# Kernel optimization log

Measured on AMD Instinct MI355X. Metric: run time of the kernel, lower is better.

## Reference

```python
import jax, jax.numpy as jnp
import numpy as np
import math

B, T, C = 2, 2048, 2048
H, KV, HD = 16, 4, 128  # num_heads, num_kv_heads, head_dim
REP = H // KV


def _rope_tables(T, hd, base=10000.0):
    inv_freq = 1.0 / (base ** (np.arange(0, hd, 2, dtype=np.float32) / hd))  # [hd/2]
    t = np.arange(T, dtype=np.float32)
    freqs = np.outer(t, inv_freq)                 # [T, hd/2]
    emb = np.concatenate([freqs, freqs], axis=-1)  # [T, hd]
    return jnp.asarray(np.cos(emb)), jnp.asarray(np.sin(emb))


def setup_inputs() -> dict:
    key = jax.random.key(0)
    ks = jax.random.split(key, 5)
    cos, sin = _rope_tables(T, HD)
    std = 0.02
    return {
        "x": jax.random.normal(ks[0], (B, T, C), dtype=jnp.float32),
        "cos": cos,
        "sin": sin,
        "Wq": jax.random.normal(ks[1], (C, H * HD), dtype=jnp.float32) * std,
        "Wk": jax.random.normal(ks[2], (C, KV * HD), dtype=jnp.float32) * std,
        "Wv": jax.random.normal(ks[3], (C, KV * HD), dtype=jnp.float32) * std,
        "Wo": jax.random.normal(ks[4], (H * HD, C), dtype=jnp.float32) * std,
    }


def _rotate_half(t):
    h = t.shape[-1] // 2
    return jnp.concatenate([-t[..., h:], t[..., :h]], axis=-1)


def reference(x, cos, sin, Wq, Wk, Wv, Wo):
    Bx, Tx, Cx = x.shape
    q = (x @ Wq).reshape(Bx, Tx, H, HD).transpose(0, 2, 1, 3)   # [B,H,T,hd]
    k = (x @ Wk).reshape(Bx, Tx, KV, HD).transpose(0, 2, 1, 3)  # [B,KV,T,hd]
    v = (x @ Wv).reshape(Bx, Tx, KV, HD).transpose(0, 2, 1, 3)
    c = cos[None, None]  # [1,1,T,hd]
    s = sin[None, None]
    q = q * c + _rotate_half(q) * s
    k = k * c + _rotate_half(k) * s
    # repeat_kv: expand KV heads to H heads (interleave within groups)
    k = jnp.repeat(k, REP, axis=1)  # [B,H,T,hd]
    v = jnp.repeat(v, REP, axis=1)
    scores = jnp.einsum("bhqd,bhkd->bhqk", q, k) / math.sqrt(HD)
    causal = jnp.triu(jnp.full((Tx, Tx), float("-inf"), dtype=scores.dtype), k=1)
    scores = jax.nn.softmax(scores + causal[None, None], axis=-1)
    out = jnp.einsum("bhqk,bhkd->bhqd", scores, v)  # [B,H,T,hd]
    out = out.transpose(0, 2, 1, 3).reshape(Bx, Tx, H * HD)
    return out @ Wo
```

## Files before the change

kernel.cpp:

```cpp
#include <hip/hip_runtime.h>
#include <hip/hip_bf16.h>
#include <math.h>

typedef __bf16 bf16_t;
typedef __bf16 bf16x8 __attribute__((ext_vector_type(8)));
typedef float f32x4 __attribute__((ext_vector_type(4)));

constexpr int Bc = 2, Tc = 2048, Cdim = 2048, Hc = 16, KVc = 4, HDc = 128;
constexpr int Mc = Bc * Tc;
constexpr int Nqkv = 3072;

typedef const __attribute__((address_space(1))) void* as1_cptr;
typedef __attribute__((address_space(3))) void* as3_ptr;

__device__ __forceinline__ void gload_lds16(const bf16_t* g, bf16_t* l) {
  __builtin_amdgcn_global_load_lds((as1_cptr)(const void*)g, (as3_ptr)(void*)l, 16, 0, 0);
}

__global__ void k_cvt_bf16(const float* __restrict__ in, bf16_t* __restrict__ out) {
  int i = (blockIdx.x * 256 + threadIdx.x) * 8;
  float4 a = *(const float4*)(in + i);
  float4 b = *(const float4*)(in + i + 4);
  bf16x8 v;
  v[0] = (bf16_t)a.x; v[1] = (bf16_t)a.y; v[2] = (bf16_t)a.z; v[3] = (bf16_t)a.w;
  v[4] = (bf16_t)b.x; v[5] = (bf16_t)b.y; v[6] = (bf16_t)b.z; v[7] = (bf16_t)b.w;
  *(bf16x8*)(out + i) = v;
}

__global__ void k_w_trans(const float* __restrict__ W, bf16_t* __restrict__ Wt,
                          int K, int N) {
  __shared__ alignas(16) bf16_t tile[64][72];
  const int k0 = blockIdx.x * 64, n0 = blockIdx.y * 64;
  const int t = threadIdx.x;
#pragma unroll
  for (int i = 0; i < 4; ++i) {
    int idx = t + i * 256;
    int r = idx >> 4;
    int c4 = (idx & 15) * 4;
    float4 v = *(const float4*)(W + (size_t)(k0 + r) * N + n0 + c4);
    tile[r][c4 + 0] = (bf16_t)v.x; tile[r][c4 + 1] = (bf16_t)v.y;
    tile[r][c4 + 2] = (bf16_t)v.z; tile[r][c4 + 3] = (bf16_t)v.w;
  }
  __syncthreads();
#pragma unroll
  for (int i = 0; i < 4; ++i) {
    int idx = t + i * 256;
    int n = idx >> 4;
    int kc = (idx & 15) * 4;
    alignas(8) bf16_t o[4];
#pragma unroll
    for (int j = 0; j < 4; ++j) o[j] = tile[kc + j][n];
    *(uint2*)(Wt + (size_t)(n0 + n) * K + k0 + kc) = *(uint2*)o;
  }
}

template <typename OutT>
__global__ __launch_bounds__(256, 2) void k_gemm_bt(
    const bf16_t* __restrict__ A, const bf16_t* __restrict__ Bt,
    OutT* __restrict__ Cout, int M, int N, int K) {
  __shared__ alignas(16) bf16_t Ash[128 * 64];
  __shared__ alignas(16) bf16_t Bsh[128 * 64];
  const int tid = threadIdx.x;
  const int wave = tid >> 6, lane = tid & 63;
  const int col = lane & 15, quad = lane >> 4;
  const int m0 = blockIdx.y * 128, n0 = blockIdx.x * 128;
  const int wr = wave >> 1, wc = wave & 1;

  f32x4 acc[4][4];
#pragma unroll
  for (int i = 0; i < 4; ++i)
#pragma unroll
    for (int j = 0; j < 4; ++j) acc[i][j] = f32x4{0.f, 0.f, 0.f, 0.f};

  const int lrow = lane >> 3;
  const int lkc8 = (lane & 7) ^ lrow;

  for (int k0 = 0; k0 < K; k0 += 64) {
    __syncthreads();
#pragma unroll
    for (int i = 0; i < 4; ++i) {
      const int rb = wave * 32 + i * 8;
      gload_lds16(A + (size_t)(m0 + rb + lrow) * K + k0 + lkc8 * 8, Ash + rb * 64);
      gload_lds16(Bt + (size_t)(n0 + rb + lrow) * K + k0 + lkc8 * 8, Bsh + rb * 64);
    }
    __syncthreads();
#pragma unroll
    for (int kc = 0; kc < 2; ++kc) {
      bf16x8 af[4], bfr[4];
#pragma unroll
      for (int mt = 0; mt < 4; ++mt) {
        const int m = wr * 64 + mt * 16 + col;
        const int slot = (kc * 4 + quad) ^ (m & 7);
        af[mt] = *(const bf16x8*)(Ash + m * 64 + slot * 8);
      }
#pragma unroll
      for (int nt = 0; nt < 4; ++nt) {
        const int n = wc * 64 + nt * 16 + col;
        const int slot = (kc * 4 + quad) ^ (n & 7);
        bfr[nt] = *(const bf16x8*)(Bsh + n * 64 + slot * 8);
      }
#pragma unroll
      for (int mt = 0; mt < 4; ++mt)
#pragma unroll
        for (int nt = 0; nt < 4; ++nt)
          acc[mt][nt] = __builtin_amdgcn_mfma_f32_16x16x32_bf16(
              af[mt], bfr[nt], acc[mt][nt], 0, 0, 0);
    }
  }
#pragma unroll
  for (int mt = 0; mt < 4; ++mt)
#pragma unroll
    for (int i = 0; i < 4; ++i) {
      const int row = m0 + wr * 64 + mt * 16 + quad * 4 + i;
#pragma unroll
      for (int nt = 0; nt < 4; ++nt)
        Cout[(size_t)row * N + n0 + wc * 64 + nt * 16 + col] = (OutT)acc[mt][nt][i];
    }
}

__global__ void k_rope2(const bf16_t* __restrict__ in, const float* __restrict__ cs,
                        const float* __restrict__ sn, bf16_t* __restrict__ outQ,
                        bf16_t* __restrict__ outK) {
  const int idx = blockIdx.x * 256 + threadIdx.x;
  const int d = idx & 63;
  const int hh = (idx >> 6) % 20;
  const int bt = idx / (64 * 20);
  const int t = bt & (Tc - 1);
  const int b = bt >> 11;
  const bool isQ = hh < 16;
  const int h = isQ ? hh : hh - 16;
  const int colb = isQ ? h * HDc : 2048 + h * HDc;
  const size_t bi = (size_t)(b * Tc + t) * Nqkv + colb;
  const float x0 = (float)in[bi + d];
  const float x1 = (float)in[bi + d + 64];
  const float c0 = cs[t * HDc + d], c1 = cs[t * HDc + d + 64];
  const float s0 = sn[t * HDc + d], s1 = sn[t * HDc + d + 64];
  bf16_t* op = isQ ? outQ + ((size_t)(b * Hc + h) * Tc + t) * HDc
                   : outK + ((size_t)(b * KVc + h) * Tc + t) * HDc;
  op[d]      = (bf16_t)(x0 * c0 - x1 * s0);
  op[d + 64] = (bf16_t)(x1 * c1 + x0 * s1);
}

__global__ void k_vtrans(const bf16_t* __restrict__ v, bf16_t* __restrict__ vt,
                         int in_stride, int col_off) {
  __shared__ alignas(16) bf16_t tile[64][136];
  const int t0 = blockIdx.x * 64;
  const int kv = blockIdx.y, b = blockIdx.z;
  const int tid = threadIdx.x;
#pragma unroll
  for (int i = 0; i < 4; ++i) {
    int idx = tid + i * 256;
    int r = idx >> 4;
    int ch = idx & 15;
    const bf16_t* gp = v + (size_t)(b * Tc + t0 + r) * in_stride + col_off + kv * HDc + ch * 8;
    *(uint4*)&tile[r][ch * 8] = *(const uint4*)gp;
  }
  __syncthreads();
#pragma unroll
  for (int i = 0; i < 4; ++i) {
    int idx = tid + i * 256;
    int d = idx >> 3;
    int tc = idx & 7;
    alignas(16) bf16_t o[8];
#pragma unroll
    for (int j = 0; j < 8; ++j) o[j] = tile[tc * 8 + j][d];
    bf16_t* gp = vt + ((size_t)(b * KVc + kv) * HDc + d) * Tc + t0 + tc * 8;
    *(uint4*)gp = *(uint4*)o;
  }
}

__global__ __launch_bounds__(256, 2) void k_attn(
    const bf16_t* __restrict__ Qp, const bf16_t* __restrict__ Kp,
    const bf16_t* __restrict__ Vt, bf16_t* __restrict__ Oout) {
  constexpr float sc2 = 0.08838834764831845f * 1.4426950408889634f;
  __shared__ alignas(16) bf16_t Ksh[2][64 * 128];
  __shared__ alignas(16) bf16_t Vsh[2][128 * 64];
  __shared__ alignas(16) bf16_t Psh[4][16 * 64];

  const int i2 = blockIdx.x, h = blockIdx.y, b = blockIdx.z;
  const int kvh = h >> 2;
  const int tid = threadIdx.x, wave = tid >> 6, lane = tid & 63;
  const int col = lane & 15, quad = lane >> 4;

  const bf16_t* Kb = Kp + (size_t)(b * KVc + kvh) * Tc * HDc;
  const bf16_t* Vb = Vt + (size_t)(b * KVc + kvh) * HDc * Tc;
  const bf16_t* Qbh = Qp + (size_t)(b * Hc + h) * Tc * HDc;

  const int st_kr = lane >> 4, st_kc8 = lane & 15;
  const int st_vr = lane >> 3, st_vc8 = lane & 7;

  const int qb0 = 31 - i2, qb1 = i2;
  const int n0it = qb0 + 1;
  const int ntot = qb0 + qb1 + 2;

  int q0 = qb0 * 64 + wave * 16;

  bf16x8 qf[4];
  {
    const bf16_t* qbase = Qbh + (size_t)(q0 + col) * HDc;
#pragma unroll
    for (int kc = 0; kc < 4; ++kc) {
      bf16x8 raw = *(const bf16x8*)(qbase + kc * 32 + quad * 8);
#pragma unroll
      for (int e = 0; e < 8; ++e) qf[kc][e] = (bf16_t)((float)raw[e] * sc2);
    }
  }

  f32x4 o_acc[8];
#pragma unroll
  for (int nb = 0; nb < 8; ++nb) o_acc[nb] = f32x4{0.f, 0.f, 0.f, 0.f};
  float l_i[4] = {0.f, 0.f, 0.f, 0.f};

#pragma unroll
  for (int i = 0; i < 4; ++i) {
    const int rb = wave * 16 + i * 4;
    const int r = rb + st_kr;
    const int kc8 = st_kc8 ^ (r & 7);
    gload_lds16(Kb + (size_t)r * HDc + kc8 * 8, &Ksh[0][rb * 128]);
    const int db = wave * 32 + i * 8;
    const int d = db + st_vr;
    const int tc8 = st_vc8 ^ (d & 7);
    gload_lds16(Vb + (size_t)d * Tc + tc8 * 8, &Vsh[0][db * 64]);
  }

#pragma unroll 1
  for (int j = 0; j < ntot; ++j) {
    const int cur = j & 1;
    const bool diag = (j == qb0) || (j == ntot - 1);
    asm volatile("s_barrier" ::: "memory");
    {
      const int jn = (j + 1 < ntot) ? (j + 1) : (ntot - 1);
      const int tn = (jn < n0it) ? jn : (jn - n0it);
      const int kbn = tn * 64;
#pragma unroll
      for (int i = 0; i < 4; ++i) {
        const int rb = wave * 16 + i * 4;
        const int r = rb + st_kr;
        const int kc8 = st_kc8 ^ (r & 7);
        gload_lds16(Kb + (size_t)(kbn + r) * HDc + kc8 * 8, &Ksh[cur ^ 1][rb * 128]);
        const int db = wave * 32 + i * 8;
        const int d = db + st_vr;
        const int tc8 = st_vc8 ^ (d & 7);
        gload_lds16(Vb + (size_t)d * Tc + kbn + tc8 * 8, &Vsh[cur ^ 1][db * 64]);
      }
    }
    asm volatile("s_waitcnt vmcnt(8)" ::: "memory");
    asm volatile("s_barrier" ::: "memory");

    const bf16_t* Kc = &Ksh[cur][0];
    const bf16_t* Vc = &Vsh[cur][0];

    f32x4 st[4];
#pragma unroll
    for (int tb = 0; tb < 4; ++tb) st[tb] = f32x4{0.f, 0.f, 0.f, 0.f};
#pragma unroll
    for (int kc = 0; kc < 4; ++kc)
#pragma unroll
      for (int tb = 0; tb < 4; ++tb) {
        const int r = tb * 16 + col;
        const int slot = (kc * 4 + quad) ^ (r & 7);
        bf16x8 kf = *(const bf16x8*)(Kc + r * 128 + slot * 8);
        st[tb] = __builtin_amdgcn_mfma_f32_16x16x32_bf16(qf[kc], kf, st[tb], 0, 0, 0);
      }

    bf16_t* pw = &Psh[wave][0];
    const int rowthr = wave * 16 + quad * 4;
#pragma unroll
    for (int i = 0; i < 4; ++i) {
      float e0 = exp2f(st[0][i]), e1 = exp2f(st[1][i]);
      float e2 = exp2f(st[2][i]), e3 = exp2f(st[3][i]);
      if (diag) {
        const int thr = rowthr + i;
        if (col      > thr) e0 = 0.f;
        if (16 + col > thr) e1 = 0.f;
        if (32 + col > thr) e2 = 0.f;
        if (48 + col > thr) e3 = 0.f;
      }
      l_i[i] += (e0 + e1) + (e2 + e3);
      const int r7 = (quad * 4 + i) & 7;
      const int rbase = (quad * 4 + i) * 64;
      const int c7 = col & 7, ch = col >> 3;
      pw[rbase + ((ch    ) ^ r7) * 8 + c7] = (bf16_t)e0;
      pw[rbase + ((ch + 2) ^ r7) * 8 + c7] = (bf16_t)e1;
      pw[rbase + ((ch + 4) ^ r7) * 8 + c7] = (bf16_t)e2;
      pw[rbase + ((ch + 6) ^ r7) * 8 + c7] = (bf16_t)e3;
    }
    asm volatile("s_waitcnt lgkmcnt(0)" ::: "memory");

#pragma unroll
    for (int kc = 0; kc < 2; ++kc) {
      const int slot = ((kc * 4) + quad) ^ (col & 7);
      const bf16x8 pf = *(const bf16x8*)(pw + col * 64 + slot * 8);
#pragma unroll
      for (int nb = 0; nb < 8; ++nb) {
        const int d = nb * 16 + col;
        const int vslot = (kc * 4 + quad) ^ (d & 7);
        bf16x8 vf = *(const bf16x8*)(Vc + d * 64 + vslot * 8);
        o_acc[nb] = __builtin_amdgcn_mfma_f32_16x16x32_bf16(pf, vf, o_acc[nb], 0, 0, 0);
      }
    }

    if (j == qb0) {
#pragma unroll
      for (int i = 0; i < 4; ++i) {
        float rs = l_i[i];
        rs += __shfl_xor(rs, 1);
        rs += __shfl_xor(rs, 2);
        rs += __shfl_xor(rs, 4);
        rs += __shfl_xor(rs, 8);
        const float inv = 1.0f / rs;
        const int qrow = q0 + quad * 4 + i;
        bf16_t* op = Oout + ((size_t)(b * Tc) + qrow) * (Hc * HDc) + h * HDc;
#pragma unroll
        for (int nb = 0; nb < 8; ++nb) op[nb * 16 + col] = (bf16_t)(o_acc[nb][i] * inv);
        l_i[i] = 0.f;
      }
#pragma unroll
      for (int nb = 0; nb < 8; ++nb) o_acc[nb] = f32x4{0.f, 0.f, 0.f, 0.f};
      q0 = qb1 * 64 + wave * 16;
      const bf16_t* qbase = Qbh + (size_t)(q0 + col) * HDc;
#pragma unroll
      for (int kc = 0; kc < 4; ++kc) {
        bf16x8 raw = *(const bf16x8*)(qbase + kc * 32 + quad * 8);
#pragma unroll
        for (int e = 0; e < 8; ++e) qf[kc][e] = (bf16_t)((float)raw[e] * sc2);
      }
    }
  }

#pragma unroll
  for (int i = 0; i < 4; ++i) {
    float rs = l_i[i];
    rs += __shfl_xor(rs, 1);
    rs += __shfl_xor(rs, 2);
    rs += __shfl_xor(rs, 4);
    rs += __shfl_xor(rs, 8);
    const float inv = 1.0f / rs;
    const int qrow = q0 + quad * 4 + i;
    bf16_t* op = Oout + ((size_t)(b * Tc) + qrow) * (Hc * HDc) + h * HDc;
#pragma unroll
    for (int nb = 0; nb < 8; ++nb) op[nb * 16 + col] = (bf16_t)(o_acc[nb][i] * inv);
  }
}

extern "C" void kernel_launch(void* const* d_in, const int* in_sizes, int n_in,
                              void* d_out, int out_size, void* d_ws, size_t ws_size,
                              hipStream_t stream) {
  (void)in_sizes; (void)n_in; (void)out_size; (void)ws_size;
  const float* x    = (const float*)d_in[0];
  const float* cosT = (const float*)d_in[1];
  const float* sinT = (const float*)d_in[2];
  const float* Wq   = (const float*)d_in[3];
  const float* Wk   = (const float*)d_in[4];
  const float* Wv   = (const float*)d_in[5];
  const float* Wo   = (const float*)d_in[6];
  float* out = (float*)d_out;

  char* ws = (char*)d_ws;
  size_t off = 0;
  auto take = [&](size_t bytes) { char* p = ws + off; off += (bytes + 255) & ~(size_t)255; return p; };

  bf16_t* xb    = (bf16_t*)take((size_t)Mc * Cdim * 2);
  bf16_t* Wqkvt = (bf16_t*)take((size_t)Nqkv * Cdim * 2);
  bf16_t* Wot   = (bf16_t*)take((size_t)Cdim * (Hc * HDc) * 2);
  bf16_t* qkv   = (bf16_t*)take((size_t)Mc * Nqkv * 2);
  bf16_t* Kp    = (bf16_t*)take((size_t)Mc * (KVc * HDc) * 2);
  bf16_t* Vt    = (bf16_t*)take((size_t)Mc * (KVc * HDc) * 2);
  bf16_t* Wqt = Wqkvt;
  bf16_t* Wkt = Wqkvt + (size_t)2048 * Cdim;
  bf16_t* Wvt = Wqkvt + (size_t)2560 * Cdim;
  bf16_t* Qp   = xb;
  bf16_t* attn = qkv;

  k_cvt_bf16<<<dim3((Mc * Cdim) / 2048), dim3(256), 0, stream>>>(x, xb);
  k_w_trans<<<dim3(Cdim / 64, 2048 / 64), dim3(256), 0, stream>>>(Wq, Wqt, Cdim, 2048);
  k_w_trans<<<dim3(Cdim / 64, 512 / 64), dim3(256), 0, stream>>>(Wk, Wkt, Cdim, 512);
  k_w_trans<<<dim3(Cdim / 64, 512 / 64), dim3(256), 0, stream>>>(Wv, Wvt, Cdim, 512);
  k_w_trans<<<dim3((Hc * HDc) / 64, Cdim / 64), dim3(256), 0, stream>>>(Wo, Wot, Hc * HDc, Cdim);
  k_gemm_bt<bf16_t><<<dim3(Nqkv / 128, Mc / 128), dim3(256), 0, stream>>>(
      xb, Wqkvt, qkv, Mc, Nqkv, Cdim);
  k_rope2<<<dim3((Bc * Tc * 20 * 64) / 256), dim3(256), 0, stream>>>(
      qkv, cosT, sinT, Qp, Kp);
  k_vtrans<<<dim3(Tc / 64, KVc, Bc), dim3(256), 0, stream>>>(qkv, Vt, Nqkv, 2560);
  k_attn<<<dim3(16, Hc, Bc), dim3(256), 0, stream>>>(Qp, Kp, Vt, attn);
  k_gemm_bt<float><<<dim3(Cdim / 128, Mc / 128), dim3(256), 0, stream>>>(
      attn, Wot, out, Mc, Cdim, Hc * HDc);
}
```

Baseline: 308.9 us.

## Restructure attention to 8-wave blocks sharing K/V tiles across two query tiles

The attention kernel drops the paired front/back query-tile scheme. Each block now runs 512 threads covering one 128-row query tile, with two 4-wave groups sharing each K/V LDS tile, so each K/V tile is loaded once for twice as many query rows. Load balance comes from reversing the tile order for batch 1, and the group that has passed its diagonal sits idle in later iterations. The three QKV weight transposes are merged into one launch, and the GEMM launch bounds are raised to 3 blocks per CU, which may add register pressure.

```diff
diff --git a/kernel.cpp b/kernel.cpp
--- a/kernel.cpp
+++ b/kernel.cpp
@@ -27,6 +27,37 @@
   *(bf16x8*)(out + i) = v;
 }
 
+__global__ void k_wqkv_trans(const float* __restrict__ Wq, const float* __restrict__ Wk,
+                             const float* __restrict__ Wv, bf16_t* __restrict__ Wt) {
+  __shared__ alignas(16) bf16_t tile[64][72];
+  const int k0 = blockIdx.x * 64, n0 = blockIdx.y * 64;
+  const float* src; int srcN, ncol0;
+  if (n0 < 2048)      { src = Wq; srcN = 2048; ncol0 = n0; }
+  else if (n0 < 2560) { src = Wk; srcN = 512;  ncol0 = n0 - 2048; }
+  else                { src = Wv; srcN = 512;  ncol0 = n0 - 2560; }
+  const int t = threadIdx.x;
+#pragma unroll
+  for (int i = 0; i < 4; ++i) {
+    int idx = t + i * 256;
+    int r = idx >> 4;
+    int c4 = (idx & 15) * 4;
+    float4 v = *(const float4*)(src + (size_t)(k0 + r) * srcN + ncol0 + c4);
+    tile[r][c4 + 0] = (bf16_t)v.x; tile[r][c4 + 1] = (bf16_t)v.y;
+    tile[r][c4 + 2] = (bf16_t)v.z; tile[r][c4 + 3] = (bf16_t)v.w;
+  }
+  __syncthreads();
+#pragma unroll
+  for (int i = 0; i < 4; ++i) {
+    int idx = t + i * 256;
+    int n = idx >> 4;
+    int kc = (idx & 15) * 4;
+    alignas(8) bf16_t o[4];
+#pragma unroll
+    for (int j = 0; j < 4; ++j) o[j] = tile[kc + j][n];
+    *(uint2*)(Wt + (size_t)(n0 + n) * Cdim + k0 + kc) = *(uint2*)o;
+  }
+}
+
 __global__ void k_w_trans(const float* __restrict__ W, bf16_t* __restrict__ Wt,
                           int K, int N) {
   __shared__ alignas(16) bf16_t tile[64][72];
@@ -55,7 +86,7 @@
 }
 
 template <typename OutT>
-__global__ __launch_bounds__(256, 2) void k_gemm_bt(
+__global__ __launch_bounds__(256, 3) void k_gemm_bt(
     const bf16_t* __restrict__ A, const bf16_t* __restrict__ Bt,
     OutT* __restrict__ Cout, int M, int N, int K) {
   __shared__ alignas(16) bf16_t Ash[128 * 64];
@@ -169,18 +200,24 @@
   }
 }
 
-__global__ __launch_bounds__(256, 2) void k_attn(
+__global__ __launch_bounds__(512, 2) void k_attn(
     const bf16_t* __restrict__ Qp, const bf16_t* __restrict__ Kp,
     const bf16_t* __restrict__ Vt, bf16_t* __restrict__ Oout) {
   constexpr float sc2 = 0.08838834764831845f * 1.4426950408889634f;
   __shared__ alignas(16) bf16_t Ksh[2][64 * 128];
   __shared__ alignas(16) bf16_t Vsh[2][128 * 64];
-  __shared__ alignas(16) bf16_t Psh[4][16 * 64];
-
-  const int i2 = blockIdx.x, h = blockIdx.y, b = blockIdx.z;
+  __shared__ alignas(16) bf16_t Psh[8][16 * 64];
+
+  const int h = blockIdx.y, b = blockIdx.z;
+  const int qt = b ? (15 - blockIdx.x) : blockIdx.x;
   const int kvh = h >> 2;
   const int tid = threadIdx.x, wave = tid >> 6, lane = tid & 63;
+  const int grp = wave >> 2, wsub = wave & 3;
   const int col = lane & 15, quad = lane >> 4;
+  const int q0 = qt * 128 + grp * 64 + wsub * 16;
+
+  const int dtile = 2 * qt + grp;
+  const int niter = 2 * qt + 2;
 
   const bf16_t* Kb = Kp + (size_t)(b * KVc + kvh) * Tc * HDc;
   const bf16_t* Vb = Vt + (size_t)(b * KVc + kvh) * HDc * Tc;
@@ -189,12 +226,6 @@
   const int st_kr = lane >> 4, st_kc8 = lane & 15;
   const int st_vr = lane >> 3, st_vc8 = lane & 7;
 
-  const int qb0 = 31 - i2, qb1 = i2;
-  const int n0it = qb0 + 1;
-  const int ntot = qb0 + qb1 + 2;
-
-  int q0 = qb0 * 64 + wave * 16;
-
   bf16x8 qf[4];
   {
     const bf16_t* qbase = Qbh + (size_t)(q0 + col) * HDc;
@@ -212,121 +243,96 @@
   float l_i[4] = {0.f, 0.f, 0.f, 0.f};
 
 #pragma unroll
-  for (int i = 0; i < 4; ++i) {
-    const int rb = wave * 16 + i * 4;
+  for (int i = 0; i < 2; ++i) {
+    const int rb = wave * 8 + i * 4;
     const int r = rb + st_kr;
     const int kc8 = st_kc8 ^ (r & 7);
     gload_lds16(Kb + (size_t)r * HDc + kc8 * 8, &Ksh[0][rb * 128]);
-    const int db = wave * 32 + i * 8;
+    const int db = wave * 16 + i * 8;
     const int d = db + st_vr;
     const int tc8 = st_vc8 ^ (d & 7);
     gload_lds16(Vb + (size_t)d * Tc + tc8 * 8, &Vsh[0][db * 64]);
   }
 
 #pragma unroll 1
-  for (int j = 0; j < ntot; ++j) {
+  for (int j = 0; j < niter; ++j) {
     const int cur = j & 1;
-    const bool diag = (j == qb0) || (j == ntot - 1);
     asm volatile("s_barrier" ::: "memory");
     {
-      const int jn = (j + 1 < ntot) ? (j + 1) : (ntot - 1);
-      const int tn = (jn < n0it) ? jn : (jn - n0it);
-      const int kbn = tn * 64;
-#pragma unroll
-      for (int i = 0; i < 4; ++i) {
-        const int rb = wave * 16 + i * 4;
+      const int jn = (j + 1 < niter) ? (j + 1) : (niter - 1);
+      const int kbn = jn * 64;
+#pragma unroll
+      for (int i = 0; i < 2; ++i) {
+        const int rb = wave * 8 + i * 4;
         const int r = rb + st_kr;
         const int kc8 = st_kc8 ^ (r & 7);
         gload_lds16(Kb + (size_t)(kbn + r) * HDc + kc8 * 8, &Ksh[cur ^ 1][rb * 128]);
-        const int db = wave * 32 + i * 8;
+        const int db = wave * 16 + i * 8;
         const int d = db + st_vr;
         const int tc8 = st_vc8 ^ (d & 7);
         gload_lds16(Vb + (size_t)d * Tc + kbn + tc8 * 8, &Vsh[cur ^ 1][db * 64]);
       }
     }
-    asm volatile("s_waitcnt vmcnt(8)" ::: "memory");
+    asm volatile("s_waitcnt vmcnt(4)" ::: "memory");
     asm volatile("s_barrier" ::: "memory");
 
-    const bf16_t* Kc = &Ksh[cur][0];
-    const bf16_t* Vc = &Vsh[cur][0];
-
-    f32x4 st[4];
-#pragma unroll
-    for (int tb = 0; tb < 4; ++tb) st[tb] = f32x4{0.f, 0.f, 0.f, 0.f};
-#pragma unroll
-    for (int kc = 0; kc < 4; ++kc)
-#pragma unroll
-      for (int tb = 0; tb < 4; ++tb) {
-        const int r = tb * 16 + col;
-        const int slot = (kc * 4 + quad) ^ (r & 7);
-        bf16x8 kf = *(const bf16x8*)(Kc + r * 128 + slot * 8);
-        st[tb] = __builtin_amdgcn_mfma_f32_16x16x32_bf16(qf[kc], kf, st[tb], 0, 0, 0);
-      }
-
-    bf16_t* pw = &Psh[wave][0];
-    const int rowthr = wave * 16 + quad * 4;
-#pragma unroll
-    for (int i = 0; i < 4; ++i) {
-      float e0 = exp2f(st[0][i]), e1 = exp2f(st[1][i]);
-      float e2 = exp2f(st[2][i]), e3 = exp2f(st[3][i]);
-      if (diag) {
-        const int thr = rowthr + i;
-        if (col      > thr) e0 = 0.f;
-        if (16 + col > thr) e1 = 0.f;
-        if (32 + col > thr) e2 = 0.f;
-        if (48 + col > thr) e3 = 0.f;
-      }
-      l_i[i] += (e0 + e1) + (e2 + e3);
-      const int r7 = (quad * 4 + i) & 7;
-      const int rbase = (quad * 4 + i) * 64;
-      const int c7 = col & 7, ch = col >> 3;
-      pw[rbase + ((ch    ) ^ r7) * 8 + c7] = (bf16_t)e0;
-      pw[rbase + ((ch + 2) ^ r7) * 8 + c7] = (bf16_t)e1;
-      pw[rbase + ((ch + 4) ^ r7) * 8 + c7] = (bf16_t)e2;
-      pw[rbase + ((ch + 6) ^ r7) * 8 + c7] = (bf16_t)e3;
-    }
-    asm volatile("s_waitcnt lgkmcnt(0)" ::: "memory");
-
-#pragma unroll
-    for (int kc = 0; kc < 2; ++kc) {
-      const int slot = ((kc * 4) + quad) ^ (col & 7);
-      const bf16x8 pf = *(const bf16x8*)(pw + col * 64 + slot * 8);
-#pragma unroll
-      for (int nb = 0; nb < 8; ++nb) {
-        const int d = nb * 16 + col;
-        const int vslot = (kc * 4 + quad) ^ (d & 7);
-        bf16x8 vf = *(const bf16x8*)(Vc + d * 64 + vslot * 8);
-        o_acc[nb] = __builtin_amdgcn_mfma_f32_16x16x32_bf16(pf, vf, o_acc[nb], 0, 0, 0);
-      }
-    }
-
-    if (j == qb0) {
+    if (j <= dtile) {
+      const bool diag = (j == dtile);
+      const bf16_t* Kc = &Ksh[cur][0];
+      const bf16_t* Vc = &Vsh[cur][0];
+
+      f32x4 st[4];
+#pragma unroll
+      for (int tb = 0; tb < 4; ++tb) st[tb] = f32x4{0.f, 0.f, 0.f, 0.f};
+#pragma unroll
+      for (int kc = 0; kc < 4; ++kc)
+#pragma unroll
+        for (int tb = 0; tb < 4; ++tb) {
+          const int r = tb * 16 + col;
+          const int slot = (kc * 4 + quad) ^ (r & 7);
+          bf16x8 kf = *(const bf16x8*)(Kc + r * 128 + slot * 8);
+          st[tb] = __builtin_amdgcn_mfma_f32_16x16x32_bf16(qf[kc], kf, st[tb], 0, 0, 0);
+        }
+
+      bf16_t* pw = &Psh[wave][0];
+      const int rowthr = wsub * 16 + quad * 4;
 #pragma unroll
       for (int i = 0; i < 4; ++i) {
-        float rs = l_i[i];
-        rs += __shfl_xor(rs, 1);
-        rs += __shfl_xor(rs, 2);
-        rs += __shfl_xor(rs, 4);
-        rs += __shfl_xor(rs, 8);
-        const float inv = 1.0f / rs;
-        const int qrow = q0 + quad * 4 + i;
-        bf16_t* op = Oout + ((size_t)(b * Tc) + qrow) * (Hc * HDc) + h * HDc;
-#pragma unroll
-        for (int nb = 0; nb < 8; ++nb) op[nb * 16 + col] = (bf16_t)(o_acc[nb][i] * inv);
-        l_i[i] = 0.f;
-      }
-#pragma unroll
-      for (int nb = 0; nb < 8; ++nb) o_acc[nb] = f32x4{0.f, 0.f, 0.f, 0.f};
-      q0 = qb1 * 64 + wave * 16;
-      const bf16_t* qbase = Qbh + (size_t)(q0 + col) * HDc;
-#pragma unroll
-      for (int kc = 0; kc < 4; ++kc) {
-        bf16x8 raw = *(const bf16x8*)(qbase + kc * 32 + quad * 8);
-#pragma unroll
-        for (int e = 0; e < 8; ++e) qf[kc][e] = (bf16_t)((float)raw[e] * sc2);
-      }
-    }
-  }
+        float e0 = exp2f(st[0][i]), e1 = exp2f(st[1][i]);
+        float e2 = exp2f(st[2][i]), e3 = exp2f(st[3][i]);
+        if (diag) {
+          const int thr = rowthr + i;
+          if (col      > thr) e0 = 0.f;
+          if (16 + col > thr) e1 = 0.f;
+          if (32 + col > thr) e2 = 0.f;
+          if (48 + col > thr) e3 = 0.f;
+        }
+        l_i[i] += (e0 + e1) + (e2 + e3);
+        const int r7 = (quad * 4 + i) & 7;
+        const int rbase = (quad * 4 + i) * 64;
+        const int c7 = col & 7, ch = col >> 3;
+        pw[rbase + ((ch    ) ^ r7) * 8 + c7] = (bf16_t)e0;
+        pw[rbase + ((ch + 2) ^ r7) * 8 + c7] = (bf16_t)e1;
+        pw[rbase + ((ch + 4) ^ r7) * 8 + c7] = (bf16_t)e2;
+        pw[rbase + ((ch + 6) ^ r7) * 8 + c7] = (bf16_t)e3;
+      }
+      asm volatile("s_waitcnt lgkmcnt(0)" ::: "memory");
+
+#pragma unroll
+      for (int kc = 0; kc < 2; ++kc) {
+        const int slot = ((kc * 4) + quad) ^ (col & 7);
+        const bf16x8 pf = *(const bf16x8*)(pw + col * 64 + slot * 8);
+#pragma unroll
+        for (int nb = 0; nb < 8; ++nb) {
+          const int d = nb * 16 + col;
+          const int vslot = (kc * 4 + quad) ^ (d & 7);
+          bf16x8 vf = *(const bf16x8*)(Vc + d * 64 + vslot * 8);
+          o_acc[nb] = __builtin_amdgcn_mfma_f32_16x16x32_bf16(pf, vf, o_acc[nb], 0, 0, 0);
+        }
+      }
+    }
+  }
+  asm volatile("s_waitcnt vmcnt(0)" ::: "memory");
 
 #pragma unroll
   for (int i = 0; i < 4; ++i) {
@@ -366,23 +372,18 @@
   bf16_t* qkv   = (bf16_t*)take((size_t)Mc * Nqkv * 2);
   bf16_t* Kp    = (bf16_t*)take((size_t)Mc * (KVc * HDc) * 2);
   bf16_t* Vt    = (bf16_t*)take((size_t)Mc * (KVc * HDc) * 2);
-  bf16_t* Wqt = Wqkvt;
-  bf16_t* Wkt = Wqkvt + (size_t)2048 * Cdim;
-  bf16_t* Wvt = Wqkvt + (size_t)2560 * Cdim;
   bf16_t* Qp   = xb;
   bf16_t* attn = qkv;
 
   k_cvt_bf16<<<dim3((Mc * Cdim) / 2048), dim3(256), 0, stream>>>(x, xb);
-  k_w_trans<<<dim3(Cdim / 64, 2048 / 64), dim3(256), 0, stream>>>(Wq, Wqt, Cdim, 2048);
-  k_w_trans<<<dim3(Cdim / 64, 512 / 64), dim3(256), 0, stream>>>(Wk, Wkt, Cdim, 512);
-  k_w_trans<<<dim3(Cdim / 64, 512 / 64), dim3(256), 0, stream>>>(Wv, Wvt, Cdim, 512);
+  k_wqkv_trans<<<dim3(Cdim / 64, Nqkv / 64), dim3(256), 0, stream>>>(Wq, Wk, Wv, Wqkvt);
   k_w_trans<<<dim3((Hc * HDc) / 64, Cdim / 64), dim3(256), 0, stream>>>(Wo, Wot, Hc * HDc, Cdim);
   k_gemm_bt<bf16_t><<<dim3(Nqkv / 128, Mc / 128), dim3(256), 0, stream>>>(
       xb, Wqkvt, qkv, Mc, Nqkv, Cdim);
   k_rope2<<<dim3((Bc * Tc * 20 * 64) / 256), dim3(256), 0, stream>>>(
       qkv, cosT, sinT, Qp, Kp);
   k_vtrans<<<dim3(Tc / 64, KVc, Bc), dim3(256), 0, stream>>>(qkv, Vt, Nqkv, 2560);
-  k_attn<<<dim3(16, Hc, Bc), dim3(256), 0, stream>>>(Qp, Kp, Vt, attn);
+  k_attn<<<dim3(16, Hc, Bc), dim3(512), 0, stream>>>(Qp, Kp, Vt, attn);
   k_gemm_bt<float><<<dim3(Cdim / 128, Mc / 128), dim3(256), 0, stream>>>(
       attn, Wot, out, Mc, Cdim, Hc * HDc);
 }
```

Result: slower. 347.0 us (+12.4%).
